# Kernel tuning notes

Measured on AMD Instinct MI355X. Metric: run time of the kernel, lower is better.

Reference implementation:

```python
import jax, jax.numpy as jnp
import numpy as np

B, S, D_MODEL, D_K, D_V, H = 2, 2048, 1024, 1024, 1024, 16


def setup_inputs() -> dict:
    key = jax.random.key(0)
    ks = jax.random.split(key, 12)
    s = 0.02
    inp = {
        "queries": jax.random.normal(ks[0], (B, S, D_MODEL), jnp.float32),
        "keys": jax.random.normal(ks[1], (B, S, D_MODEL), jnp.float32),
        "values": jax.random.normal(ks[2], (B, S, D_MODEL), jnp.float32),
        # causal mask: 1 where attention is disallowed (added as -1e9*mask)
        "mask": jnp.triu(jnp.ones((1, 1, S, S), jnp.float32), k=1),
        "Wq": jax.random.normal(ks[3], (D_MODEL, D_K), jnp.float32) * s,
        "bq": jnp.zeros((D_K,), jnp.float32),
        "Wk": jax.random.normal(ks[4], (D_MODEL, D_K), jnp.float32) * s,
        "bk": jnp.zeros((D_K,), jnp.float32),
        "Wv": jax.random.normal(ks[5], (D_MODEL, D_V), jnp.float32) * s,
        "bv": jnp.zeros((D_V,), jnp.float32),
        "Wo": jax.random.normal(ks[6], (D_K, D_MODEL), jnp.float32) * s,
        "bo": jnp.zeros((D_MODEL,), jnp.float32),
    }
    return inp


def _split_heads(x):  # [B,S,D] -> [B,H,S,D/H]
    b, s, d = x.shape
    return x.reshape(b, s, H, d // H).transpose(0, 2, 1, 3)


def reference(queries, keys, values, mask, Wq, bq, Wk, bk, Wv, bv, Wo, bo):
    q = _split_heads(queries @ Wq + bq)   # [B,H,S,hd]
    k = _split_heads(keys @ Wk + bk)
    v = _split_heads(values @ Wv + bv)
    # NOTE: original scales by sqrt(full d_k), not per-head dim (faithful quirk)
    scores = jnp.einsum("bhqd,bhkd->bhqk", q, k) / jnp.sqrt(jnp.float32(D_K))
    scores = scores + (-1e9) * mask
    w = jax.nn.softmax(scores, axis=-1)
    out = jnp.einsum("bhqk,bhkd->bhqd", w, v)        # [B,H,S,hd]
    out = out.transpose(0, 2, 1, 3).reshape(q.shape[0], q.shape[2], D_K)
    return out @ Wo + bo
```

## Files before the change

kernel.cpp:

```cpp
#include <hip/hip_runtime.h>
#include <hip/hip_bf16.h>
#include <cstdint>

typedef __bf16 bf16;
typedef __bf16 bf16x2 __attribute__((ext_vector_type(2)));
typedef __bf16 bf16x4 __attribute__((ext_vector_type(4)));
typedef __bf16 bf16x8 __attribute__((ext_vector_type(8)));
typedef float f32x4 __attribute__((ext_vector_type(4)));
typedef float f32x16 __attribute__((ext_vector_type(16)));
typedef unsigned int u32;

#define B_ 2
#define S_ 2048
#define DM 1024
#define H_ 16
#define HD 64

__device__ __forceinline__ void gload_lds16(const bf16* g, bf16* l) {
  __builtin_amdgcn_global_load_lds((const __attribute__((address_space(1))) void*)g,
                                   (__attribute__((address_space(3))) void*)l,
                                   16, 0, 0);
}

__device__ __forceinline__ u32 cvt_pk_bf16(float lo, float hi) {
  u32 r;
  asm("v_cvt_pk_bf16_f32 %0, %1, %2" : "=v"(r) : "v"(lo), "v"(hi));
  return r;
}

__global__ __launch_bounds__(256) void convert_k(const float* __restrict__ s0,
                                                 const float* __restrict__ s1,
                                                 const float* __restrict__ s2,
                                                 bf16* __restrict__ d0,
                                                 bf16* __restrict__ d1,
                                                 bf16* __restrict__ d2) {
  const float* s = (blockIdx.z == 0) ? s0 : (blockIdx.z == 1) ? s1 : s2;
  bf16* d = (blockIdx.z == 0) ? d0 : (blockIdx.z == 1) ? d1 : d2;
  const size_t i = ((size_t)blockIdx.x * 256 + threadIdx.x) * 8;
  f32x4 a = *(const f32x4*)(s + i);
  f32x4 b = *(const f32x4*)(s + i + 4);
  bf16x8 o;
#pragma unroll
  for (int j = 0; j < 4; j++) { o[j] = (bf16)a[j]; o[j + 4] = (bf16)b[j]; }
  *(bf16x8*)(d + i) = o;
}

__global__ __launch_bounds__(256) void transposeW_k(
    const float* __restrict__ w0, const float* __restrict__ w1,
    const float* __restrict__ w2, const float* __restrict__ w3,
    bf16* __restrict__ t0, bf16* __restrict__ t1,
    bf16* __restrict__ t2, bf16* __restrict__ t3) {
  const float* src = (blockIdx.z == 0) ? w0 : (blockIdx.z == 1) ? w1
                     : (blockIdx.z == 2) ? w2 : w3;
  bf16* dst = (blockIdx.z == 0) ? t0 : (blockIdx.z == 1) ? t1
              : (blockIdx.z == 2) ? t2 : t3;
  __shared__ float tile[32][33];
  const int tx = threadIdx.x, ty = threadIdx.y;
  const int x0 = blockIdx.x * 32, y0 = blockIdx.y * 32;
#pragma unroll
  for (int r = 0; r < 4; r++)
    tile[ty + r * 8][tx] = src[(size_t)(y0 + ty + r * 8) * DM + x0 + tx];
  __syncthreads();
#pragma unroll
  for (int r = 0; r < 4; r++)
    dst[(size_t)(x0 + ty + r * 8) * DM + y0 + tx] = (bf16)tile[tx][ty + r * 8];
}

struct GArgs { const void* A; const bf16* Bt; const float* bias; void* C; };
struct GArgs3 { GArgs g[3]; };

__global__ __launch_bounds__(512, 2) void gemm256_k(GArgs3 args, int M, int N,
                                                    int K, int tilesY, int tilesX) {
  const int nwg = gridDim.x;
  const int id = blockIdx.x;
  const int wgid = (id & 7) * (nwg >> 3) + (id >> 3);
  const int perz = tilesY * tilesX;
  const int z = wgid / perz;
  const int rem = wgid - z * perz;
  const int ty = rem / tilesX, tx = rem - (rem / tilesX) * tilesX;
  const GArgs ga = args.g[z];
  const int m0 = ty * 256, n0 = tx * 256;

  __shared__ __align__(16) bf16 As[2][16384];
  __shared__ __align__(16) bf16 Bs[2][16384];

  const int tid = threadIdx.x;
  const int lane = tid & 63, w = tid >> 6;
  const int l15 = lane & 15, q = lane >> 4;
  const int wr = w >> 2, wc = w & 3;

  const bf16* gA[4];
  const bf16* gB[4];
#pragma unroll
  for (int i = 0; i < 4; i++) {
    const int ci = i * 512 + w * 64 + lane;
    const int row = ci >> 3, ch = ci & 7, sc = ch ^ (row & 7);
    gA[i] = (const bf16*)ga.A + (size_t)(m0 + row) * K + sc * 8;
    gB[i] = ga.Bt + (size_t)(n0 + row) * K + sc * 8;
  }

  const int cA0 = ((q) ^ (l15 & 7)) * 8;
  const int cA1 = ((4 + q) ^ (l15 & 7)) * 8;

  f32x4 acc[8][4] = {};

#pragma unroll
  for (int i = 0; i < 4; i++) {
    gload_lds16(gA[i], &As[0][(i * 512 + w * 64) * 8]);
    gload_lds16(gB[i], &Bs[0][(i * 512 + w * 64) * 8]);
  }
  asm volatile("s_waitcnt vmcnt(0)" ::: "memory");
  __builtin_amdgcn_s_barrier();

  const int NT = K >> 6;
  for (int t = 0; t < NT; ++t) {
    const int cur = t & 1;
    const bf16* Ac = As[cur];
    const bf16* Bc = Bs[cur];

    bf16x8 a[4][2], b[2][2][2];
#pragma unroll
    for (int mt = 0; mt < 4; mt++) {
      const int row = wr * 128 + mt * 16 + l15;
      a[mt][0] = *(const bf16x8*)(Ac + row * 64 + cA0);
      a[mt][1] = *(const bf16x8*)(Ac + row * 64 + cA1);
    }
#pragma unroll
    for (int nt = 0; nt < 2; nt++) {
      const int row = wc * 64 + nt * 16 + l15;
      b[0][nt][0] = *(const bf16x8*)(Bc + row * 64 + cA0);
      b[0][nt][1] = *(const bf16x8*)(Bc + row * 64 + cA1);
    }
    if (t + 1 < NT) {
      const int k0 = (t + 1) << 6;
      bf16* An = As[cur ^ 1];
      bf16* Bn = Bs[cur ^ 1];
#pragma unroll
      for (int i = 0; i < 4; i++) {
        gload_lds16(gA[i] + k0, An + (i * 512 + w * 64) * 8);
        gload_lds16(gB[i] + k0, Bn + (i * 512 + w * 64) * 8);
      }
    }
    __builtin_amdgcn_s_setprio(1);
#pragma unroll
    for (int mt = 0; mt < 4; mt++)
#pragma unroll
      for (int nt = 0; nt < 2; nt++)
#pragma unroll
        for (int kk = 0; kk < 2; kk++)
          acc[mt][nt] = __builtin_amdgcn_mfma_f32_16x16x32_bf16(
              a[mt][kk], b[0][nt][kk], acc[mt][nt], 0, 0, 0);
    __builtin_amdgcn_s_setprio(0);
    __builtin_amdgcn_s_barrier();

#pragma unroll
    for (int nt = 0; nt < 2; nt++) {
      const int row = wc * 64 + 32 + nt * 16 + l15;
      b[1][nt][0] = *(const bf16x8*)(Bc + row * 64 + cA0);
      b[1][nt][1] = *(const bf16x8*)(Bc + row * 64 + cA1);
    }
    __builtin_amdgcn_s_setprio(1);
#pragma unroll
    for (int mt = 0; mt < 4; mt++)
#pragma unroll
      for (int nt = 0; nt < 2; nt++)
#pragma unroll
        for (int kk = 0; kk < 2; kk++)
          acc[mt][2 + nt] = __builtin_amdgcn_mfma_f32_16x16x32_bf16(
              a[mt][kk], b[1][nt][kk], acc[mt][2 + nt], 0, 0, 0);
    __builtin_amdgcn_s_setprio(0);
    __builtin_amdgcn_s_barrier();

#pragma unroll
    for (int mt = 0; mt < 4; mt++) {
      const int row = wr * 128 + 64 + mt * 16 + l15;
      a[mt][0] = *(const bf16x8*)(Ac + row * 64 + cA0);
      a[mt][1] = *(const bf16x8*)(Ac + row * 64 + cA1);
    }
    __builtin_amdgcn_s_setprio(1);
#pragma unroll
    for (int mt = 0; mt < 4; mt++)
#pragma unroll
      for (int nt = 0; nt < 2; nt++)
#pragma unroll
        for (int kk = 0; kk < 2; kk++)
          acc[4 + mt][2 + nt] = __builtin_amdgcn_mfma_f32_16x16x32_bf16(
              a[mt][kk], b[1][nt][kk], acc[4 + mt][2 + nt], 0, 0, 0);
    __builtin_amdgcn_s_setprio(0);
    __builtin_amdgcn_s_barrier();

    __builtin_amdgcn_s_setprio(1);
#pragma unroll
    for (int mt = 0; mt < 4; mt++)
#pragma unroll
      for (int nt = 0; nt < 2; nt++)
#pragma unroll
        for (int kk = 0; kk < 2; kk++)
          acc[4 + mt][nt] = __builtin_amdgcn_mfma_f32_16x16x32_bf16(
              a[mt][kk], b[0][nt][kk], acc[4 + mt][nt], 0, 0, 0);
    __builtin_amdgcn_s_setprio(0);
    asm volatile("s_waitcnt vmcnt(0)" ::: "memory");
    __builtin_amdgcn_s_barrier();
  }

#pragma unroll
  for (int nh = 0; nh < 2; nh++)
#pragma unroll
    for (int nt = 0; nt < 2; nt++) {
      const int col = n0 + wc * 64 + nh * 32 + nt * 16 + l15;
      const float bv = ga.bias[col];
#pragma unroll
      for (int mh = 0; mh < 2; mh++)
#pragma unroll
        for (int mt = 0; mt < 4; mt++) {
          const int row = m0 + wr * 128 + mh * 64 + mt * 16 + q * 4;
          f32x4 v = acc[mh * 4 + mt][nh * 2 + nt];
#pragma unroll
          for (int r = 0; r < 4; r++)
            ((bf16*)ga.C)[(size_t)(row + r) * N + col] = (bf16)(v[r] + bv);
        }
    }
}

template <bool AF32, bool CF32>
__global__ __launch_bounds__(256) void gemm_k(GArgs3 args, int M, int N, int K) {
  const GArgs ga = args.g[blockIdx.z];
  __shared__ __align__(16) bf16 As[128 * 32];
  __shared__ __align__(16) bf16 Bs[128 * 32];
  const int tid = threadIdx.x;
  const int lane = tid & 63, w = tid >> 6;
  const int l15 = lane & 15, q = lane >> 4;
  const int wr = w >> 1, wc = w & 1;

  int bx = blockIdx.x, by = blockIdx.y;
  if constexpr (CF32) {
    const int nb = gridDim.x * gridDim.y;
    const int id = by * gridDim.x + bx;
    const int wg = (id & 7) * (nb >> 3) + (id >> 3);
    bx = wg % gridDim.x;
    by = wg / gridDim.x;
  }
  const int m0 = by * 128, n0 = bx * 128;

  const int c0 = w * 128 + lane;
  const int c1 = c0 + 64;
  const int r0 = c0 >> 2, r1 = c1 >> 2, koff = (c0 & 3) * 8;
  const bf16* gB0 = ga.Bt + (size_t)(n0 + r0) * K + koff;
  const bf16* gB1 = ga.Bt + (size_t)(n0 + r1) * K + koff;
  bf16* lA0 = As + (w * 2 + 0) * 512;
  bf16* lA1 = As + (w * 2 + 1) * 512;
  bf16* lB0 = Bs + (w * 2 + 0) * 512;
  bf16* lB1 = Bs + (w * 2 + 1) * 512;

  const float* pA0 = nullptr;
  const float* pA1 = nullptr;
  f32x4 t00, t01, t10, t11;
  if constexpr (AF32) {
    const float* A = (const float*)ga.A;
    pA0 = A + (size_t)(m0 + r0) * K + koff;
    pA1 = A + (size_t)(m0 + r1) * K + koff;
    t00 = *(const f32x4*)pA0; t01 = *(const f32x4*)(pA0 + 4);
    t10 = *(const f32x4*)pA1; t11 = *(const f32x4*)(pA1 + 4);
  }

  f32x4 acc[4][4] = {};

  for (int k0 = 0; k0 < K; k0 += 32) {
    if constexpr (AF32) {
      bf16x8 va0, va1;
#pragma unroll
      for (int j = 0; j < 4; j++) {
        va0[j] = (bf16)t00[j]; va0[j + 4] = (bf16)t01[j];
        va1[j] = (bf16)t10[j]; va1[j + 4] = (bf16)t11[j];
      }
      *(bf16x8*)(lA0 + lane * 8) = va0;
      *(bf16x8*)(lA1 + lane * 8) = va1;
    } else {
      const bf16* A = (const bf16*)ga.A;
      gload_lds16(A + (size_t)(m0 + r0) * K + koff + k0, lA0);
      gload_lds16(A + (size_t)(m0 + r1) * K + koff + k0, lA1);
    }
    gload_lds16(gB0 + k0, lB0);
    gload_lds16(gB1 + k0, lB1);
    __syncthreads();

    bf16x8 a[4], b[4];
#pragma unroll
    for (int mt = 0; mt < 4; mt++)
      a[mt] = *(const bf16x8*)(As + (wr * 64 + mt * 16 + l15) * 32 + q * 8);
#pragma unroll
    for (int nt = 0; nt < 4; nt++)
      b[nt] = *(const bf16x8*)(Bs + (wc * 64 + nt * 16 + l15) * 32 + q * 8);

    if constexpr (AF32) {
      const int kn = (k0 + 32 < K) ? k0 + 32 : k0;
      t00 = *(const f32x4*)(pA0 + kn); t01 = *(const f32x4*)(pA0 + kn + 4);
      t10 = *(const f32x4*)(pA1 + kn); t11 = *(const f32x4*)(pA1 + kn + 4);
    }

#pragma unroll
    for (int mt = 0; mt < 4; mt++)
#pragma unroll
      for (int nt = 0; nt < 4; nt++)
        acc[mt][nt] = __builtin_amdgcn_mfma_f32_16x16x32_bf16(a[mt], b[nt],
                                                              acc[mt][nt], 0, 0, 0);
    __syncthreads();
  }

#pragma unroll
  for (int nt = 0; nt < 4; nt++) {
    const int col = n0 + wc * 64 + nt * 16 + l15;
    const float bv = ga.bias[col];
#pragma unroll
    for (int mt = 0; mt < 4; mt++) {
      const int row = m0 + wr * 64 + mt * 16 + q * 4;
#pragma unroll
      for (int r = 0; r < 4; r++) {
        const float val = acc[mt][nt][r] + bv;
        if constexpr (CF32)
          ((float*)ga.C)[(size_t)(row + r) * N + col] = val;
        else
          ((bf16*)ga.C)[(size_t)(row + r) * N + col] = (bf16)val;
      }
    }
  }
}

__global__ __launch_bounds__(256, 4) void attn_k(const bf16* __restrict__ Qp,
                                                 const bf16* __restrict__ Kp,
                                                 const bf16* __restrict__ Vp,
                                                 bf16* __restrict__ Op) {
  const int g = blockIdx.x;
  const int xcd = g & 7, s = g >> 3;
  const int gl = s & 3, tau = s >> 2;
  const int bh = xcd * 4 + gl;
  const int b = bh >> 4, h = bh & 15;
  const int o3 = tau & 7, hq = tau >> 3;
  const int xt = (hq == 0) ? o3 : (hq == 1) ? 15 - o3
                 : (hq == 2) ? 16 + o3 : 31 - o3;
  const int i0 = xt * 64;

  const int tid = threadIdx.x;
  const int lane = tid & 63, w = tid >> 6;
  const int l31 = lane & 31, hi = lane >> 5;
  const int qh = w >> 1, kh = w & 1;

  __shared__ __align__(16) char smem[33280];
  bf16 (*Ks)[64][64] = (bf16 (*)[64][64])smem;
  bf16 (*Vts)[64][64] = (bf16 (*)[64][64])(smem + 16384);

  const size_t headoff = (size_t)b * S_ * DM + h * HD;
  const bf16* Kb = Kp + headoff;
  const bf16* Vb = Vp + headoff;

  const int kr0 = tid >> 3, kr1 = 32 + (tid >> 3), kcb = (tid & 7) * 8;
  const int cK = ((tid & 7) ^ (kr0 & 7)) * 8;
  const int d0 = (tid & 31) * 2, kq = (tid >> 5) * 8;
  const int cV0 = ((tid >> 5) ^ (d0 & 7)) * 8;
  const int cV1 = ((tid >> 5) ^ ((d0 + 1) & 7)) * 8;
  const float QSCALE = 0.04508422f;

  bf16x8 qreg[4];
  {
    const bf16* qb = Qp + headoff + (size_t)(i0 + qh * 32 + l31) * DM + hi * 8;
#pragma unroll
    for (int kk = 0; kk < 4; kk++) {
      bf16x8 v = *(const bf16x8*)(qb + kk * 16);
      bf16x8 o;
#pragma unroll
      for (int j = 0; j < 8; j++) o[j] = (bf16)((float)v[j] * QSCALE);
      qreg[kk] = o;
    }
  }

  const int NI = (i0 >> 6) + 1;

  bf16x8 kR0 = *(const bf16x8*)(Kb + (size_t)kr0 * DM + kcb);
  bf16x8 kR1 = *(const bf16x8*)(Kb + (size_t)kr1 * DM + kcb);
  bf16x2 vR[8];
#pragma unroll
  for (int j = 0; j < 8; j++)
    vR[j] = *(const bf16x2*)(Vb + (size_t)(kq + j) * DM + d0);
  *(bf16x8*)&Ks[0][kr0][cK] = kR0;
  *(bf16x8*)&Ks[0][kr1][cK] = kR1;
  {
    bf16x8 vlo, vhi;
#pragma unroll
    for (int j = 0; j < 8; j++) { vlo[j] = vR[j][0]; vhi[j] = vR[j][1]; }
    *(bf16x8*)&Vts[0][d0][cV0] = vlo;
    *(bf16x8*)&Vts[0][d0 + 1][cV1] = vhi;
  }
  if (NI > 1) {
    kR0 = *(const bf16x8*)(Kb + (size_t)(64 + kr0) * DM + kcb);
    kR1 = *(const bf16x8*)(Kb + (size_t)(64 + kr1) * DM + kcb);
#pragma unroll
    for (int j = 0; j < 8; j++)
      vR[j] = *(const bf16x2*)(Vb + (size_t)(64 + kq + j) * DM + d0);
  }
  __syncthreads();

  f32x16 oacc0 = {}, oacc1 = {};
  float rsum = 0.f;
  int buf = 0;

  for (int t = 0; t < NI; ++t, buf ^= 1) {
    if (t + 1 < NI) {
      *(bf16x8*)&Ks[buf ^ 1][kr0][cK] = kR0;
      *(bf16x8*)&Ks[buf ^ 1][kr1][cK] = kR1;
      bf16x8 vlo, vhi;
#pragma unroll
      for (int j = 0; j < 8; j++) { vlo[j] = vR[j][0]; vhi[j] = vR[j][1]; }
      *(bf16x8*)&Vts[buf ^ 1][d0][cV0] = vlo;
      *(bf16x8*)&Vts[buf ^ 1][d0 + 1][cV1] = vhi;
    }
    if (t + 2 < NI) {
      const size_t jn = (size_t)(t + 2) * 64;
      kR0 = *(const bf16x8*)(Kb + (jn + kr0) * DM + kcb);
      kR1 = *(const bf16x8*)(Kb + (jn + kr1) * DM + kcb);
#pragma unroll
      for (int j = 0; j < 8; j++)
        vR[j] = *(const bf16x2*)(Vb + (jn + kq + j) * DM + d0);
    }

    const bool diag = (t == NI - 1);
    if (!(diag && kh > qh)) {
      f32x16 sa = {}, sb = {};
      __builtin_amdgcn_s_setprio(1);
#pragma unroll
      for (int kk = 0; kk < 2; kk++) {
        bf16x8 ka = *(const bf16x8*)
            &Ks[buf][kh * 32 + l31][((2 * kk + hi) ^ (l31 & 7)) * 8];
        sa = __builtin_amdgcn_mfma_f32_32x32x16_bf16(ka, qreg[kk], sa, 0, 0, 0);
      }
#pragma unroll
      for (int kk = 2; kk < 4; kk++) {
        bf16x8 ka = *(const bf16x8*)
            &Ks[buf][kh * 32 + l31][((2 * kk + hi) ^ (l31 & 7)) * 8];
        sb = __builtin_amdgcn_mfma_f32_32x32x16_bf16(ka, qreg[kk], sb, 0, 0, 0);
      }
      __builtin_amdgcn_s_setprio(0);

      float p[16];
      if (diag) {
        const int qrl = qh * 32 + l31;
#pragma unroll
        for (int r = 0; r < 16; r++) {
          const int keyl = kh * 32 + (r & 3) + 8 * (r >> 2) + 4 * hi;
          p[r] = (keyl <= qrl) ? __builtin_amdgcn_exp2f(sa[r] + sb[r]) : 0.f;
        }
      } else {
#pragma unroll
        for (int r = 0; r < 16; r++)
          p[r] = __builtin_amdgcn_exp2f(sa[r] + sb[r]);
      }
      {
        float q0 = (p[0] + p[1]) + (p[2] + p[3]);
        float q1 = (p[4] + p[5]) + (p[6] + p[7]);
        float q2 = (p[8] + p[9]) + (p[10] + p[11]);
        float q3 = (p[12] + p[13]) + (p[14] + p[15]);
        rsum += (q0 + q1) + (q2 + q3);
      }

      u32 Aq[4][2];
#pragma unroll
      for (int t2 = 0; t2 < 4; t2++) {
        Aq[t2][0] = cvt_pk_bf16(p[4 * t2 + 0], p[4 * t2 + 1]);
        Aq[t2][1] = cvt_pk_bf16(p[4 * t2 + 2], p[4 * t2 + 3]);
      }
      bf16x8 pb[2];
#pragma unroll
      for (int s2 = 0; s2 < 2; s2++) {
        auto e0 = __builtin_amdgcn_permlane32_swap(Aq[2 * s2][0], Aq[2 * s2 + 1][0], false, false);
        auto e1 = __builtin_amdgcn_permlane32_swap(Aq[2 * s2][1], Aq[2 * s2 + 1][1], false, false);
        union { u32 u[4]; bf16x8 v; } cv;
        cv.u[0] = e0[0]; cv.u[1] = e1[0]; cv.u[2] = e0[1]; cv.u[3] = e1[1];
        pb[s2] = cv.v;
      }

      __builtin_amdgcn_s_setprio(1);
#pragma unroll
      for (int s2 = 0; s2 < 2; s2++) {
        const int cv = ((kh * 4 + s2 * 2 + hi) ^ (l31 & 7)) * 8;
        bf16x8 va0 = *(const bf16x8*)&Vts[buf][l31][cv];
        bf16x8 va1 = *(const bf16x8*)&Vts[buf][32 + l31][cv];
        oacc0 = __builtin_amdgcn_mfma_f32_32x32x16_bf16(va0, pb[s2], oacc0, 0, 0, 0);
        oacc1 = __builtin_amdgcn_mfma_f32_32x32x16_bf16(va1, pb[s2], oacc1, 0, 0, 0);
      }
      __builtin_amdgcn_s_setprio(0);
    }

    __syncthreads();
  }

  float rtot_w = rsum + __shfl_xor(rsum, 32);
  float* osum = (float*)smem;
  float* auxf = (float*)(smem + 32768);
#pragma unroll
  for (int m = 0; m < 2; m++) {
#pragma unroll
    for (int rq = 0; rq < 4; rq++) {
      f32x4 v4;
#pragma unroll
      for (int e = 0; e < 4; e++)
        v4[e] = m ? oacc1[rq * 4 + e] : oacc0[rq * 4 + e];
      *(f32x4*)(osum + w * 2048 + (m * 4 + rq) * 256 + lane * 4) = v4;
    }
  }
  if (lane < 32) auxf[w * 32 + lane] = rtot_w;
  __syncthreads();

  {
    const int q = tid >> 2, q31b = q & 31, qh2 = q >> 5;
    const float rtot = auxf[(qh2 * 2 + 0) * 32 + q31b] + auxf[(qh2 * 2 + 1) * 32 + q31b];
    const float rinv = 1.0f / rtot;
    const int dbase = (tid & 3) * 16;
    bf16* orow = Op + headoff + (size_t)(i0 + q) * DM + dbase;
#pragma unroll
    for (int gg = 0; gg < 2; gg++) {
      bf16x8 o8;
#pragma unroll
      for (int e = 0; e < 8; e++) {
        const int d = dbase + gg * 8 + e;
        const int base = (((d >> 5) << 2) | ((d >> 3) & 3)) * 256 +
                         (q31b + 32 * ((d >> 2) & 1)) * 4 + (d & 3);
        const float v = osum[(qh2 * 2 + 0) * 2048 + base] +
                        osum[(qh2 * 2 + 1) * 2048 + base];
        o8[e] = (bf16)(v * rinv);
      }
      *(bf16x8*)(orow + gg * 8) = o8;
    }
  }
}

extern "C" void kernel_launch(void* const* d_in, const int* in_sizes, int n_in,
                              void* d_out, int out_size, void* d_ws, size_t ws_size,
                              hipStream_t stream) {
  const float* q_in = (const float*)d_in[0];
  const float* k_in = (const float*)d_in[1];
  const float* v_in = (const float*)d_in[2];
  const float* Wq = (const float*)d_in[4];
  const float* bq = (const float*)d_in[5];
  const float* Wk = (const float*)d_in[6];
  const float* bk = (const float*)d_in[7];
  const float* Wv = (const float*)d_in[8];
  const float* bv = (const float*)d_in[9];
  const float* Wo = (const float*)d_in[10];
  const float* bo = (const float*)d_in[11];

  bf16* ws = (bf16*)d_ws;
  const size_t NQ = (size_t)B_ * S_ * DM;
  bf16* Qp = ws;
  bf16* Kp = ws + NQ;
  bf16* Vp = ws + 2 * NQ;
  bf16* WqT = ws + 3 * NQ;
  bf16* WkT = WqT + (size_t)DM * DM;
  bf16* WvT = WkT + (size_t)DM * DM;
  bf16* WoT = WvT + (size_t)DM * DM;
  bf16* qb = WoT + (size_t)DM * DM;
  bf16* kb = qb + NQ;
  bf16* vb = kb + NQ;

  const bool fast = ws_size >= (size_t)(28 * 1024 * 1024) * 2;

  transposeW_k<<<dim3(32, 32, 4), dim3(32, 8), 0, stream>>>(
      Wq, Wk, Wv, Wo, WqT, WkT, WvT, WoT);

  if (fast) {
    convert_k<<<dim3((B_ * S_ * DM) / (256 * 8), 1, 3), 256, 0, stream>>>(
        q_in, k_in, v_in, qb, kb, vb);
    GArgs3 g3;
    g3.g[0] = {qb, WqT, bq, Qp};
    g3.g[1] = {kb, WkT, bk, Kp};
    g3.g[2] = {vb, WvT, bv, Vp};
    gemm256_k<<<dim3(192), 512, 0, stream>>>(g3, B_ * S_, DM, DM, 16, 4);
  } else {
    GArgs3 g3;
    g3.g[0] = {q_in, WqT, bq, Qp};
    g3.g[1] = {k_in, WkT, bk, Kp};
    g3.g[2] = {v_in, WvT, bv, Vp};
    gemm_k<true, false><<<dim3(DM / 128, (B_ * S_) / 128, 3), 256, 0, stream>>>(
        g3, B_ * S_, DM, DM);
  }

  attn_k<<<dim3(1024, 1, 1), 256, 0, stream>>>(Qp, Kp, Vp, Qp);

  GArgs3 gp;
  gp.g[0] = {Qp, WoT, bo, d_out};
  gp.g[1] = gp.g[0];
  gp.g[2] = gp.g[0];
  gemm_k<false, true><<<dim3(DM / 128, (B_ * S_) / 128, 1), 256, 0, stream>>>(
      gp, B_ * S_, DM, DM);
}
```

Before: 225.7 us.

## Replace 256x256 QKV GEMM with 128x256 tiles, triple-buffered LDS and staged epilogue

```diff
diff --git a/kernel.cpp b/kernel.cpp
--- a/kernel.cpp
+++ b/kernel.cpp
@@ -69,157 +69,131 @@
 struct GArgs { const void* A; const bf16* Bt; const float* bias; void* C; };
 struct GArgs3 { GArgs g[3]; };
 
-__global__ __launch_bounds__(512, 2) void gemm256_k(GArgs3 args, int M, int N,
-                                                    int K, int tilesY, int tilesX) {
+__global__ __launch_bounds__(512, 1) void gemm128_k(GArgs3 args, int M, int N,
+                                                    int K) {
+  __shared__ __align__(16) bf16 SA_[73728];
+  bf16* const SB_ = SA_ + 24576;
+
   const int nwg = gridDim.x;
   const int id = blockIdx.x;
   const int wgid = (id & 7) * (nwg >> 3) + (id >> 3);
-  const int perz = tilesY * tilesX;
-  const int z = wgid / perz;
-  const int rem = wgid - z * perz;
-  const int ty = rem / tilesX, tx = rem - (rem / tilesX) * tilesX;
+  const int z = wgid >> 7;
+  const int rem = wgid & 127;
+  const int tx = rem >> 5, ty = rem & 31;
   const GArgs ga = args.g[z];
-  const int m0 = ty * 256, n0 = tx * 256;
-
-  __shared__ __align__(16) bf16 As[2][16384];
-  __shared__ __align__(16) bf16 Bs[2][16384];
+  const int m0 = ty * 128, n0 = tx * 256;
 
   const int tid = threadIdx.x;
   const int lane = tid & 63, w = tid >> 6;
   const int l15 = lane & 15, q = lane >> 4;
   const int wr = w >> 2, wc = w & 3;
 
-  const bf16* gA[4];
+  const bf16* gA[2];
   const bf16* gB[4];
+  int dA[2], dB[4];
+#pragma unroll
+  for (int i = 0; i < 2; i++) {
+    const int ci = i * 512 + w * 64 + lane;
+    const int row = ci >> 3, sc = (ci & 7) ^ (row & 7);
+    gA[i] = (const bf16*)ga.A + (size_t)(m0 + row) * K + sc * 8;
+    dA[i] = (i * 512 + w * 64) * 8;
+  }
 #pragma unroll
   for (int i = 0; i < 4; i++) {
     const int ci = i * 512 + w * 64 + lane;
-    const int row = ci >> 3, ch = ci & 7, sc = ch ^ (row & 7);
-    gA[i] = (const bf16*)ga.A + (size_t)(m0 + row) * K + sc * 8;
+    const int row = ci >> 3, sc = (ci & 7) ^ (row & 7);
     gB[i] = ga.Bt + (size_t)(n0 + row) * K + sc * 8;
-  }
-
-  const int cA0 = ((q) ^ (l15 & 7)) * 8;
+    dB[i] = (i * 512 + w * 64) * 8;
+  }
+
+  const int cA0 = (q ^ (l15 & 7)) * 8;
   const int cA1 = ((4 + q) ^ (l15 & 7)) * 8;
 
-  f32x4 acc[8][4] = {};
-
-#pragma unroll
-  for (int i = 0; i < 4; i++) {
-    gload_lds16(gA[i], &As[0][(i * 512 + w * 64) * 8]);
-    gload_lds16(gB[i], &Bs[0][(i * 512 + w * 64) * 8]);
-  }
+  f32x4 acc[4][4] = {};
+
+  const int NT = K >> 6;
+
+#pragma unroll
+  for (int tt = 0; tt < 2; tt++) {
+    bf16* Ab = SA_ + tt * 8192;
+    bf16* Bb = SB_ + tt * 16384;
+    const int k0 = tt * 64;
+    gload_lds16(gA[0] + k0, Ab + dA[0]);
+    gload_lds16(gA[1] + k0, Ab + dA[1]);
+#pragma unroll
+    for (int i = 0; i < 4; i++) gload_lds16(gB[i] + k0, Bb + dB[i]);
+  }
+  asm volatile("s_waitcnt vmcnt(6)" ::: "memory");
+  __builtin_amdgcn_s_barrier();
+
+  for (int t = 0; t < NT; ++t) {
+    const int rb = t % 3;
+    const int wb = (t + 2) % 3;
+    const int kpre = ((t + 2 < NT) ? t + 2 : NT - 1) << 6;
+    {
+      bf16* Ab = SA_ + wb * 8192;
+      bf16* Bb = SB_ + wb * 16384;
+      gload_lds16(gA[0] + kpre, Ab + dA[0]);
+      gload_lds16(gA[1] + kpre, Ab + dA[1]);
+#pragma unroll
+      for (int i = 0; i < 4; i++) gload_lds16(gB[i] + kpre, Bb + dB[i]);
+    }
+
+    const bf16* Ab = SA_ + rb * 8192;
+    const bf16* Bb = SB_ + rb * 16384;
+    bf16x8 a[4][2], b[4][2];
+#pragma unroll
+    for (int mt = 0; mt < 4; mt++) {
+      const int ro = (wr * 64 + mt * 16 + l15) * 64;
+      a[mt][0] = *(const bf16x8*)(Ab + ro + cA0);
+      a[mt][1] = *(const bf16x8*)(Ab + ro + cA1);
+    }
+#pragma unroll
+    for (int nt = 0; nt < 4; nt++) {
+      const int ro = (wc * 64 + nt * 16 + l15) * 64;
+      b[nt][0] = *(const bf16x8*)(Bb + ro + cA0);
+      b[nt][1] = *(const bf16x8*)(Bb + ro + cA1);
+    }
+
+    __builtin_amdgcn_s_setprio(1);
+#pragma unroll
+    for (int mt = 0; mt < 4; mt++)
+#pragma unroll
+      for (int nt = 0; nt < 4; nt++)
+#pragma unroll
+        for (int kk = 0; kk < 2; kk++)
+          acc[mt][nt] = __builtin_amdgcn_mfma_f32_16x16x32_bf16(
+              a[mt][kk], b[nt][kk], acc[mt][nt], 0, 0, 0);
+    __builtin_amdgcn_s_setprio(0);
+
+    asm volatile("s_waitcnt vmcnt(6)" ::: "memory");
+    __builtin_amdgcn_s_barrier();
+  }
+
   asm volatile("s_waitcnt vmcnt(0)" ::: "memory");
   __builtin_amdgcn_s_barrier();
 
-  const int NT = K >> 6;
-  for (int t = 0; t < NT; ++t) {
-    const int cur = t & 1;
-    const bf16* Ac = As[cur];
-    const bf16* Bc = Bs[cur];
-
-    bf16x8 a[4][2], b[2][2][2];
-#pragma unroll
-    for (int mt = 0; mt < 4; mt++) {
-      const int row = wr * 128 + mt * 16 + l15;
-      a[mt][0] = *(const bf16x8*)(Ac + row * 64 + cA0);
-      a[mt][1] = *(const bf16x8*)(Ac + row * 64 + cA1);
-    }
-#pragma unroll
-    for (int nt = 0; nt < 2; nt++) {
-      const int row = wc * 64 + nt * 16 + l15;
-      b[0][nt][0] = *(const bf16x8*)(Bc + row * 64 + cA0);
-      b[0][nt][1] = *(const bf16x8*)(Bc + row * 64 + cA1);
-    }
-    if (t + 1 < NT) {
-      const int k0 = (t + 1) << 6;
-      bf16* An = As[cur ^ 1];
-      bf16* Bn = Bs[cur ^ 1];
-#pragma unroll
-      for (int i = 0; i < 4; i++) {
-        gload_lds16(gA[i] + k0, An + (i * 512 + w * 64) * 8);
-        gload_lds16(gB[i] + k0, Bn + (i * 512 + w * 64) * 8);
-      }
-    }
-    __builtin_amdgcn_s_setprio(1);
+  bf16* Ws = SA_ + w * 4352;
+#pragma unroll
+  for (int nt = 0; nt < 4; nt++) {
+    const float bv = ga.bias[n0 + wc * 64 + nt * 16 + l15];
 #pragma unroll
     for (int mt = 0; mt < 4; mt++)
 #pragma unroll
-      for (int nt = 0; nt < 2; nt++)
-#pragma unroll
-        for (int kk = 0; kk < 2; kk++)
-          acc[mt][nt] = __builtin_amdgcn_mfma_f32_16x16x32_bf16(
-              a[mt][kk], b[0][nt][kk], acc[mt][nt], 0, 0, 0);
-    __builtin_amdgcn_s_setprio(0);
-    __builtin_amdgcn_s_barrier();
-
-#pragma unroll
-    for (int nt = 0; nt < 2; nt++) {
-      const int row = wc * 64 + 32 + nt * 16 + l15;
-      b[1][nt][0] = *(const bf16x8*)(Bc + row * 64 + cA0);
-      b[1][nt][1] = *(const bf16x8*)(Bc + row * 64 + cA1);
-    }
-    __builtin_amdgcn_s_setprio(1);
-#pragma unroll
-    for (int mt = 0; mt < 4; mt++)
-#pragma unroll
-      for (int nt = 0; nt < 2; nt++)
-#pragma unroll
-        for (int kk = 0; kk < 2; kk++)
-          acc[mt][2 + nt] = __builtin_amdgcn_mfma_f32_16x16x32_bf16(
-              a[mt][kk], b[1][nt][kk], acc[mt][2 + nt], 0, 0, 0);
-    __builtin_amdgcn_s_setprio(0);
-    __builtin_amdgcn_s_barrier();
-
-#pragma unroll
-    for (int mt = 0; mt < 4; mt++) {
-      const int row = wr * 128 + 64 + mt * 16 + l15;
-      a[mt][0] = *(const bf16x8*)(Ac + row * 64 + cA0);
-      a[mt][1] = *(const bf16x8*)(Ac + row * 64 + cA1);
-    }
-    __builtin_amdgcn_s_setprio(1);
-#pragma unroll
-    for (int mt = 0; mt < 4; mt++)
-#pragma unroll
-      for (int nt = 0; nt < 2; nt++)
-#pragma unroll
-        for (int kk = 0; kk < 2; kk++)
-          acc[4 + mt][2 + nt] = __builtin_amdgcn_mfma_f32_16x16x32_bf16(
-              a[mt][kk], b[1][nt][kk], acc[4 + mt][2 + nt], 0, 0, 0);
-    __builtin_amdgcn_s_setprio(0);
-    __builtin_amdgcn_s_barrier();
-
-    __builtin_amdgcn_s_setprio(1);
-#pragma unroll
-    for (int mt = 0; mt < 4; mt++)
-#pragma unroll
-      for (int nt = 0; nt < 2; nt++)
-#pragma unroll
-        for (int kk = 0; kk < 2; kk++)
-          acc[4 + mt][nt] = __builtin_amdgcn_mfma_f32_16x16x32_bf16(
-              a[mt][kk], b[0][nt][kk], acc[4 + mt][nt], 0, 0, 0);
-    __builtin_amdgcn_s_setprio(0);
-    asm volatile("s_waitcnt vmcnt(0)" ::: "memory");
-    __builtin_amdgcn_s_barrier();
-  }
-
-#pragma unroll
-  for (int nh = 0; nh < 2; nh++)
-#pragma unroll
-    for (int nt = 0; nt < 2; nt++) {
-      const int col = n0 + wc * 64 + nh * 32 + nt * 16 + l15;
-      const float bv = ga.bias[col];
-#pragma unroll
-      for (int mh = 0; mh < 2; mh++)
-#pragma unroll
-        for (int mt = 0; mt < 4; mt++) {
-          const int row = m0 + wr * 128 + mh * 64 + mt * 16 + q * 4;
-          f32x4 v = acc[mh * 4 + mt][nh * 2 + nt];
-#pragma unroll
-          for (int r = 0; r < 4; r++)
-            ((bf16*)ga.C)[(size_t)(row + r) * N + col] = (bf16)(v[r] + bv);
-        }
-    }
+      for (int r = 0; r < 4; r++)
+        Ws[(mt * 16 + q * 4 + r) * 68 + nt * 16 + l15] =
+            (bf16)(acc[mt][nt][r] + bv);
+  }
+#pragma unroll
+  for (int p = 0; p < 8; p++) {
+    const int lr = p * 8 + (lane >> 3), c0 = (lane & 7) * 8;
+    bf16x4 lo = *(const bf16x4*)(Ws + lr * 68 + c0);
+    bf16x4 hi = *(const bf16x4*)(Ws + lr * 68 + c0 + 4);
+    bf16x8 o;
+#pragma unroll
+    for (int j = 0; j < 4; j++) { o[j] = lo[j]; o[j + 4] = hi[j]; }
+    *(bf16x8*)((bf16*)ga.C + (size_t)(m0 + wr * 64 + lr) * N + n0 + wc * 64 + c0) = o;
+  }
 }
 
 template <bool AF32, bool CF32>
@@ -572,7 +546,7 @@
     g3.g[0] = {qb, WqT, bq, Qp};
     g3.g[1] = {kb, WkT, bk, Kp};
     g3.g[2] = {vb, WvT, bv, Vp};
-    gemm256_k<<<dim3(192), 512, 0, stream>>>(g3, B_ * S_, DM, DM, 16, 4);
+    gemm128_k<<<dim3(384), 512, 0, stream>>>(g3, B_ * S_, DM, DM);
   } else {
     GArgs3 g3;
     g3.g[0] = {q_in, WqT, bq, Qp};
```

New measurement: 227.3 us. About the same (+0.7%).
